# Optimization experiments

Measured on AMD Instinct MI355X. Metric: run time of the kernel, lower is better.

The kernel has to match this reference:

```python
import jax, jax.numpy as jnp
import numpy as np

B, N, F, W, D, LAT = 512, 200, 16, 256, 5, 128
ALPHA = 0.2  # tf.nn.leaky_relu default alpha


def _he_uniform(key, shape):
    fan_in = shape[-2]
    lim = np.sqrt(6.0 / fan_in)
    return jax.random.uniform(key, shape, jnp.float32, -lim, lim)


def setup_inputs() -> dict:
    key = jax.random.key(0)
    ks = jax.random.split(key, 16)
    x = jax.random.normal(ks[0], (B, N, F), jnp.float32)
    lengths = jax.random.randint(ks[1], (B,), 1, N + 1)
    valid = (jnp.arange(N)[None, :] < lengths[:, None])[..., None]  # [B,N,1]
    x = x * valid  # zero-pad tail -> Keras Masking marks it masked
    return {
        "x": x,
        "Gamma0": _he_uniform(ks[2], (F, W)),
        "Lambda0": _he_uniform(ks[3], (F, W)),
        "Gmid": _he_uniform(ks[4], (D - 2, W, W)),
        "Lmid": _he_uniform(ks[5], (D - 2, W, W)),
        "GammaL": _he_uniform(ks[6], (W, LAT)),
        "LambdaL": _he_uniform(ks[7], (W, LAT)),
        "F0_W": _he_uniform(ks[8], (LAT, W)),
        "F0_b": jnp.zeros((W,), jnp.float32),
        "Fmid_W": _he_uniform(ks[9], (D - 1, W, W)),
        "Fmid_b": jnp.zeros((D - 1, W), jnp.float32),
        "Flast_W": _he_uniform(ks[10], (W, 2)),
        "Flast_b": jnp.zeros((2,), jnp.float32),
    }


def _lrelu(h):
    return jnp.where(h >= 0, h, ALPHA * h)


def reference(x, Gamma0, Lambda0, Gmid, Lmid, GammaL, LambdaL,
              F0_W, F0_b, Fmid_W, Fmid_b, Flast_W, Flast_b):
    # Keras Masking(mask_value=0): position is valid if any feature != 0
    maskf = jnp.any(x != 0, axis=-1, keepdims=True).astype(x.dtype)  # [B,N,1]
    denom = jnp.sum(maskf, axis=1, keepdims=True)                    # [B,1,1]

    def ds_layer(h, G, L):
        # equivariant layer: per-element projection minus broadcast masked-mean projection
        mean = jnp.sum(h * maskf, axis=1, keepdims=True) / denom     # [B,1,in]
        return h @ G - mean @ L                                      # [B,N,out]

    h = _lrelu(ds_layer(x, Gamma0, Lambda0))
    for i in range(Gmid.shape[0]):
        h = _lrelu(ds_layer(h, Gmid[i], Lmid[i]))
    h = _lrelu(ds_layer(h, GammaL, LambdaL))

    # adder (sum over valid positions)
    pooled = jnp.sum(h * maskf, axis=1)                              # [B,LAT]

    y = _lrelu(pooled @ F0_W + F0_b)
    for i in range(Fmid_W.shape[0]):
        y = _lrelu(y @ Fmid_W[i] + Fmid_b[i])
    return jax.nn.softmax(y @ Flast_W + Flast_b, axis=-1)            # [B,2]
```

## Files before the change

### kernel.cpp

```cpp
#include <hip/hip_runtime.h>
#include <hip/hip_fp16.h>
#include <stdint.h>

#define BB 512
#define NN 200
#define FF 16
#define WW 256
#define DD 5
#define LATD 128
#define ALPHA 0.2f

#define WS_NV   0
#define WS_PERM 2048
#define WS_WSF  4096

typedef _Float16 f16x8 __attribute__((ext_vector_type(8)));
typedef float f32x4 __attribute__((ext_vector_type(4)));

__device__ __forceinline__ float lrelu(float v) { return v >= 0.f ? v : ALPHA * v; }
__device__ __forceinline__ unsigned pk2(float a, float b) {
    __half2 h = __floats2half2_rn(a, b);
    return *reinterpret_cast<unsigned*>(&h);
}
__device__ __forceinline__ unsigned swz(int rl, int cb) {
    return (unsigned)(rl * 512 + cb) ^ (unsigned)((rl & 7) << 4);
}

__global__ __launch_bounds__(256) void k1_kernel(const float* __restrict__ x,
                                                 const float* __restrict__ Gmid,
                                                 const float* __restrict__ GammaL,
                                                 _Float16* __restrict__ wsf,
                                                 int* __restrict__ nv) {
    const int tid = threadIdx.x;
    if (blockIdx.x < BB) {
        __shared__ int wavecnt[4];
        const int lane = tid & 63, w = tid >> 6;
        const float* xb = x + (size_t)blockIdx.x * NN * FF;
        bool flag = false;
        if (tid < NN) {
            const float4* xr = (const float4*)(xb + tid * FF);
            float4 v0 = xr[0], v1 = xr[1], v2 = xr[2], v3 = xr[3];
            flag = (v0.x != 0.f) | (v0.y != 0.f) | (v0.z != 0.f) | (v0.w != 0.f) |
                   (v1.x != 0.f) | (v1.y != 0.f) | (v1.z != 0.f) | (v1.w != 0.f) |
                   (v2.x != 0.f) | (v2.y != 0.f) | (v2.z != 0.f) | (v2.w != 0.f) |
                   (v3.x != 0.f) | (v3.y != 0.f) | (v3.z != 0.f) | (v3.w != 0.f);
        }
        unsigned long long bal = __ballot(flag);
        if (lane == 0) wavecnt[w] = __popcll(bal);
        __syncthreads();
        if (tid == 0) nv[blockIdx.x] = wavecnt[0] + wavecnt[1] + wavecnt[2] + wavecnt[3];
        return;
    }
    int t = (int)(blockIdx.x - BB) * 256 + tid;
    if (t < 24576) {
        int layer = t / 8192, r = t % 8192;
        int a = r / 256, n = r % 256;
        const float* G = Gmid + (size_t)layer * 65536;
        f16x8 v;
#pragma unroll
        for (int j = 0; j < 8; ++j) v[j] = (_Float16)G[(8 * a + j) * 256 + n];
        int chunk = a >> 2, g = a & 3, cf = n >> 4, ln = (n & 15) + 16 * g;
        *(f16x8*)(wsf + (size_t)layer * 65536 + ((size_t)(chunk * 16 + cf) * 64 + ln) * 8) = v;
    } else if (t < 28672) {
        int r = t - 24576;
        int a = r / 128, n = r % 128;
        f16x8 v;
#pragma unroll
        for (int j = 0; j < 8; ++j) v[j] = (_Float16)GammaL[(8 * a + j) * 128 + n];
        int chunk = a >> 2, g = a & 3, cf = n >> 4, ln = (n & 15) + 16 * g;
        *(f16x8*)(wsf + 196608 + ((size_t)(chunk * 8 + cf) * 64 + ln) * 8) = v;
    }
}

__global__ __launch_bounds__(512) void rank_kernel(const int* __restrict__ nv,
                                                   int* __restrict__ perm) {
    __shared__ int nvs[512];
    const int t = threadIdx.x;
    int my = nv[t];
    nvs[t] = my;
    __syncthreads();
    int rank = 0;
    for (int b2 = 0; b2 < 512; ++b2) {
        int o = nvs[b2];
        rank += (o > my) || (o == my && b2 < t);
    }
    perm[rank] = t;
}

struct __align__(16) FusedLds {
    unsigned short tile[NN * 256];
    float xl[NN * FF];
    float g0[FF * WW];
    float mred[512];
    float csred[8][256];
    float csl[256];
    float mpj_s[256];
    float ybuf[2][256];
    float xmean[FF];
    int wavecnt[8];
};

template <int NC>
__device__ __forceinline__ void colsum_finish(FusedLds& S, const float* fs,
                                              int tid, int lane, int w) {
    constexpr int CPW = NC / 64;
    const int cg = w & 3, cl = lane & 15;
#pragma unroll
    for (int u = 0; u < CPW; ++u) {
        float s = fs[u];
        s += __shfl_xor(s, 16);
        s += __shfl_xor(s, 32);
        if (lane < 16) S.csred[w][(cg * CPW + u) * 16 + cl] = s;
    }
    __syncthreads();
    if (tid < NC) {
        const int cgb = tid / (16 * CPW);
        S.csl[tid] = S.csred[cgb][tid] + S.csred[4 + cgb][tid];
    }
    __syncthreads();
}

template <int NC>
__device__ __forceinline__ void tile_layer(FusedLds& S, const _Float16* __restrict__ wf,
                                           int Nv, int tid, int lane, int w) {
    constexpr int CPW = NC / 64;
    const int rg = w >> 2, cg = w & 3, cl = lane & 15, g = lane >> 4;
    const int RFL = (Nv + 15) >> 4;
    float fs[CPW];
#pragma unroll
    for (int u = 0; u < CPW; ++u) fs[u] = 0.f;
    for (int p0 = 0; p0 < RFL; p0 += 8) {
        f32x4 acc[4][CPW];
#pragma unroll
        for (int i = 0; i < 4; ++i)
#pragma unroll
            for (int u = 0; u < CPW; ++u)
#pragma unroll
                for (int j = 0; j < 4; ++j) acc[i][u][j] = 0.f;
        bool act[4];
        int rll[4];
#pragma unroll
        for (int i = 0; i < 4; ++i) {
            const int rf = p0 + rg + 2 * i;
            act[i] = rf < RFL;
            int rl = rf * 16 + cl;
            rll[i] = rl < Nv ? rl : Nv - 1;
        }
#pragma unroll
        for (int c = 0; c < 8; ++c) {
            f16x8 bfr[CPW];
#pragma unroll
            for (int u = 0; u < CPW; ++u)
                bfr[u] = *(const f16x8*)(wf + ((size_t)(c * (NC / 16) + cg * CPW + u) * 64 + lane) * 8);
#pragma unroll
            for (int i = 0; i < 4; ++i) {
                if (act[i]) {
                    f16x8 af = *(const f16x8*)((const char*)S.tile + swz(rll[i], c * 64 + (g << 4)));
#pragma unroll
                    for (int u = 0; u < CPW; ++u)
                        acc[i][u] = __builtin_amdgcn_mfma_f32_16x16x32_f16(af, bfr[u], acc[i][u], 0, 0, 0);
                }
            }
        }
        __syncthreads();
#pragma unroll
        for (int i = 0; i < 4; ++i) {
            if (act[i]) {
                const int rlb = (p0 + rg + 2 * i) * 16 + 4 * g;
#pragma unroll
                for (int j = 0; j < 4; ++j) {
                    const int rl = rlb + j;
                    if (rl < Nv) {
#pragma unroll
                        for (int u = 0; u < CPW; ++u) {
                            const int col = (cg * CPW + u) * 16 + cl;
                            float o = lrelu(acc[i][u][j] - S.mpj_s[col]);
                            *(_Float16*)((char*)S.tile + swz(rl, col * 2)) = (_Float16)o;
                            fs[u] += o;
                        }
                    }
                }
            }
        }
        __syncthreads();
    }
    colsum_finish<NC>(S, fs, tid, lane, w);
}

__device__ __forceinline__ void mproj_mid(FusedLds& S, const float* __restrict__ Lmid,
                                          int l, float invNv, int tid) {
    const float* L = Lmid + (size_t)l * 65536;
    const int c = tid & 255, seg = tid >> 8;
    float a = 0.f;
    const float* Lp = L + (size_t)seg * 128 * 256 + c;
    const float* mh = S.csl + seg * 128;
#pragma unroll 8
    for (int k = 0; k < 128; ++k) a = fmaf(mh[k], Lp[(size_t)k * 256], a);
    S.mred[seg * 256 + c] = a;
    __syncthreads();
    if (tid < 256) S.mpj_s[tid] = (S.mred[tid] + S.mred[256 + tid]) * invNv;
    __syncthreads();
}

__device__ __forceinline__ void mproj_last(FusedLds& S, const float* __restrict__ LambdaL,
                                           float invNv, int tid) {
    const int c = tid & 127, seg = tid >> 7;
    float a = 0.f;
    const float* Lp = LambdaL + (size_t)seg * 64 * 128 + c;
    const float* mh = S.csl + seg * 64;
#pragma unroll 8
    for (int k = 0; k < 64; ++k) a = fmaf(mh[k], Lp[(size_t)k * 128], a);
    S.mred[seg * 128 + c] = a;
    __syncthreads();
    if (tid < 128)
        S.mpj_s[tid] = (S.mred[tid] + S.mred[128 + tid] + S.mred[256 + tid] + S.mred[384 + tid]) * invNv;
    __syncthreads();
}

__global__ __launch_bounds__(512, 2) void fused_kernel(
    const float* __restrict__ x,
    const float* __restrict__ Gamma0, const float* __restrict__ Lambda0,
    const float* __restrict__ Lmid, const float* __restrict__ LambdaL,
    const float* __restrict__ F0W, const float* __restrict__ F0b,
    const float* __restrict__ FmidW, const float* __restrict__ Fmidb,
    const float* __restrict__ FlastW, const float* __restrict__ Flastb,
    const int* __restrict__ perm, const _Float16* __restrict__ wsf,
    float* __restrict__ out) {
    __shared__ FusedLds S;
    const int tid = threadIdx.x, lane = tid & 63, w = tid >> 6;
    const int b = perm[blockIdx.x];
    const float* xb = x + (size_t)b * NN * FF;

    ((float4*)S.g0)[tid] = ((const float4*)Gamma0)[tid];
    ((float4*)S.g0)[tid + 512] = ((const float4*)Gamma0)[tid + 512];
    float4 v0, v1, v2, v3;
    bool flag = false;
    if (tid < NN) {
        const float4* xr = (const float4*)(xb + tid * FF);
        v0 = xr[0]; v1 = xr[1]; v2 = xr[2]; v3 = xr[3];
        flag = (v0.x != 0.f) | (v0.y != 0.f) | (v0.z != 0.f) | (v0.w != 0.f) |
               (v1.x != 0.f) | (v1.y != 0.f) | (v1.z != 0.f) | (v1.w != 0.f) |
               (v2.x != 0.f) | (v2.y != 0.f) | (v2.z != 0.f) | (v2.w != 0.f) |
               (v3.x != 0.f) | (v3.y != 0.f) | (v3.z != 0.f) | (v3.w != 0.f);
    }
    unsigned long long bal = __ballot(flag);
    if (lane == 0) S.wavecnt[w] = __popcll(bal);
    {
        int n0 = tid >> 4, f = tid & 15;
        float a = 0.f;
        for (int n = n0; n < NN; n += 32) a += xb[n * FF + f];
        S.mred[n0 * 16 + f] = a;
    }
    __syncthreads();
    int basec = 0, tot = 0;
#pragma unroll
    for (int w2 = 0; w2 < 8; ++w2) {
        int c = S.wavecnt[w2];
        if (w2 < w) basec += c;
        tot += c;
    }
    const int Nv = tot;
    const float invNv = 1.0f / (float)Nv;
    if (flag) {
        int pos = basec + __popcll(bal & ((1ull << lane) - 1ull));
        float4* dst = (float4*)&S.xl[pos * FF];
        dst[0] = v0; dst[1] = v1; dst[2] = v2; dst[3] = v3;
    }
    if (tid < FF) {
        float s = 0.f;
#pragma unroll
        for (int g2 = 0; g2 < 32; ++g2) s += S.mred[g2 * 16 + tid];
        S.xmean[tid] = s * invNv;
    }
    __syncthreads();
    if (tid < WW) {
        float a = 0.f;
#pragma unroll
        for (int f = 0; f < FF; ++f) a = fmaf(S.xmean[f], Lambda0[f * WW + tid], a);
        S.mpj_s[tid] = a;
    }
    __syncthreads();

    {
        const float4 mp = *(const float4*)&S.mpj_s[4 * lane];
        float p[4] = {0.f, 0.f, 0.f, 0.f};
        for (int r = w; r < Nv; r += 8) {
            float acc[4] = {0.f, 0.f, 0.f, 0.f};
#pragma unroll
            for (int f = 0; f < FF; ++f) {
                float xv = S.xl[r * FF + f];
                float4 gv = *(const float4*)&S.g0[f * WW + 4 * lane];
                acc[0] = fmaf(xv, gv.x, acc[0]);
                acc[1] = fmaf(xv, gv.y, acc[1]);
                acc[2] = fmaf(xv, gv.z, acc[2]);
                acc[3] = fmaf(xv, gv.w, acc[3]);
            }
            float o0 = lrelu(acc[0] - mp.x), o1 = lrelu(acc[1] - mp.y);
            float o2 = lrelu(acc[2] - mp.z), o3 = lrelu(acc[3] - mp.w);
            uint2 ov;
            ov.x = pk2(o0, o1);
            ov.y = pk2(o2, o3);
            *(uint2*)((char*)S.tile + swz(r, 8 * lane)) = ov;
            p[0] += o0; p[1] += o1; p[2] += o2; p[3] += o3;
        }
        __syncthreads();
#pragma unroll
        for (int c4 = 0; c4 < 4; ++c4) S.csred[w][4 * lane + c4] = p[c4];
        __syncthreads();
        if (tid < 256) {
            float s = 0.f;
#pragma unroll
            for (int w2 = 0; w2 < 8; ++w2) s += S.csred[w2][tid];
            S.csl[tid] = s;
        }
        __syncthreads();
    }

    for (int l = 0; l < DD - 2; ++l) {
        mproj_mid(S, Lmid, l, invNv, tid);
        tile_layer<256>(S, wsf + (size_t)l * 65536, Nv, tid, lane, w);
    }
    mproj_last(S, LambdaL, invNv, tid);
    tile_layer<128>(S, wsf + 196608, Nv, tid, lane, w);

    {
        const int c = tid & 255, seg = tid >> 8;
        float a = 0.f;
        const float* Wp = F0W + (size_t)seg * 64 * WW + c;
        const float* ip = S.csl + seg * 64;
#pragma unroll
        for (int k = 0; k < 64; ++k) a = fmaf(ip[k], Wp[(size_t)k * WW], a);
        S.mred[seg * WW + c] = a;
        __syncthreads();
        if (tid < WW) S.ybuf[0][tid] = lrelu(S.mred[tid] + S.mred[WW + tid] + F0b[tid]);
        __syncthreads();
    }
    int cur = 0;
    for (int i = 0; i < DD - 1; ++i) {
        const int c = tid & 255, seg = tid >> 8;
        const float* Wp = FmidW + (size_t)i * WW * WW + (size_t)seg * 128 * WW + c;
        const float* ip = S.ybuf[cur] + seg * 128;
        float a = 0.f;
#pragma unroll
        for (int k = 0; k < 128; ++k) a = fmaf(ip[k], Wp[(size_t)k * WW], a);
        S.mred[seg * WW + c] = a;
        __syncthreads();
        if (tid < WW)
            S.ybuf[1 - cur][tid] = lrelu(S.mred[tid] + S.mred[WW + tid] + Fmidb[i * WW + tid]);
        __syncthreads();
        cur = 1 - cur;
    }
    if (w == 0) {
        float s0 = 0.f, s1 = 0.f;
        for (int k = lane; k < WW; k += 64) {
            float yv = S.ybuf[cur][k];
            s0 = fmaf(yv, FlastW[2 * k], s0);
            s1 = fmaf(yv, FlastW[2 * k + 1], s1);
        }
#pragma unroll
        for (int off = 32; off > 0; off >>= 1) {
            s0 += __shfl_down(s0, off);
            s1 += __shfl_down(s1, off);
        }
        if (lane == 0) {
            s0 += Flastb[0];
            s1 += Flastb[1];
            float m = fmaxf(s0, s1);
            float e0 = expf(s0 - m), e1 = expf(s1 - m);
            float inv = 1.0f / (e0 + e1);
            out[2 * b] = e0 * inv;
            out[2 * b + 1] = e1 * inv;
        }
    }
}

extern "C" void kernel_launch(void* const* d_in, const int* in_sizes, int n_in,
                              void* d_out, int out_size, void* d_ws, size_t ws_size,
                              hipStream_t stream) {
    const float* x = (const float*)d_in[0];
    const float* Gamma0 = (const float*)d_in[1];
    const float* Lambda0 = (const float*)d_in[2];
    const float* Gmid = (const float*)d_in[3];
    const float* Lmid = (const float*)d_in[4];
    const float* GammaL = (const float*)d_in[5];
    const float* LambdaL = (const float*)d_in[6];
    const float* F0W = (const float*)d_in[7];
    const float* F0b = (const float*)d_in[8];
    const float* FmidW = (const float*)d_in[9];
    const float* Fmidb = (const float*)d_in[10];
    const float* FlastW = (const float*)d_in[11];
    const float* Flastb = (const float*)d_in[12];
    float* out = (float*)d_out;

    int* nvb = (int*)((char*)d_ws + WS_NV);
    int* perm = (int*)((char*)d_ws + WS_PERM);
    _Float16* wsf = (_Float16*)((char*)d_ws + WS_WSF);

    k1_kernel<<<BB + 112, 256, 0, stream>>>(x, Gmid, GammaL, wsf, nvb);
    rank_kernel<<<1, 512, 0, stream>>>(nvb, perm);
    fused_kernel<<<BB, 512, 0, stream>>>(x, Gamma0, Lambda0, Lmid, LambdaL,
                                         F0W, F0b, FmidW, Fmidb, FlastW, Flastb,
                                         perm, wsf, out);
}
```

Measured before the change: 147.8 us.

## Double fused block to 1024 threads and cover all rows in one MFMA pass

```diff
diff --git a/kernel.cpp b/kernel.cpp
--- a/kernel.cpp
+++ b/kernel.cpp
@@ -9,6 +9,7 @@
 #define DD 5
 #define LATD 128
 #define ALPHA 0.2f
+#define NT 1024
 
 #define WS_NV   0
 #define WS_PERM 2048
@@ -89,15 +90,16 @@
 
 struct __align__(16) FusedLds {
     unsigned short tile[NN * 256];
-    float xl[NN * FF];
-    float g0[FF * WW];
-    float mred[512];
-    float csred[8][256];
+    union U {
+        struct { float xl[NN * FF]; float g0[FF * WW]; } p;
+        float csred[16][256];
+    } u;
+    float mred[1024];
     float csl[256];
     float mpj_s[256];
     float ybuf[2][256];
     float xmean[FF];
-    int wavecnt[8];
+    int wavecnt[16];
 };
 
 template <int NC>
@@ -110,12 +112,13 @@
         float s = fs[u];
         s += __shfl_xor(s, 16);
         s += __shfl_xor(s, 32);
-        if (lane < 16) S.csred[w][(cg * CPW + u) * 16 + cl] = s;
+        if (lane < 16) S.u.csred[w][(cg * CPW + u) * 16 + cl] = s;
     }
     __syncthreads();
     if (tid < NC) {
         const int cgb = tid / (16 * CPW);
-        S.csl[tid] = S.csred[cgb][tid] + S.csred[4 + cgb][tid];
+        S.csl[tid] = S.u.csred[cgb][tid] + S.u.csred[4 + cgb][tid] +
+                     S.u.csred[8 + cgb][tid] + S.u.csred[12 + cgb][tid];
     }
     __syncthreads();
 }
@@ -129,60 +132,57 @@
     float fs[CPW];
 #pragma unroll
     for (int u = 0; u < CPW; ++u) fs[u] = 0.f;
-    for (int p0 = 0; p0 < RFL; p0 += 8) {
-        f32x4 acc[4][CPW];
-#pragma unroll
-        for (int i = 0; i < 4; ++i)
-#pragma unroll
-            for (int u = 0; u < CPW; ++u)
-#pragma unroll
-                for (int j = 0; j < 4; ++j) acc[i][u][j] = 0.f;
-        bool act[4];
-        int rll[4];
-#pragma unroll
-        for (int i = 0; i < 4; ++i) {
-            const int rf = p0 + rg + 2 * i;
-            act[i] = rf < RFL;
-            int rl = rf * 16 + cl;
-            rll[i] = rl < Nv ? rl : Nv - 1;
-        }
-#pragma unroll
-        for (int c = 0; c < 8; ++c) {
-            f16x8 bfr[CPW];
-#pragma unroll
-            for (int u = 0; u < CPW; ++u)
-                bfr[u] = *(const f16x8*)(wf + ((size_t)(c * (NC / 16) + cg * CPW + u) * 64 + lane) * 8);
-#pragma unroll
-            for (int i = 0; i < 4; ++i) {
-                if (act[i]) {
-                    f16x8 af = *(const f16x8*)((const char*)S.tile + swz(rll[i], c * 64 + (g << 4)));
-#pragma unroll
-                    for (int u = 0; u < CPW; ++u)
-                        acc[i][u] = __builtin_amdgcn_mfma_f32_16x16x32_f16(af, bfr[u], acc[i][u], 0, 0, 0);
-                }
-            }
-        }
-        __syncthreads();
+    f32x4 acc[4][CPW];
+#pragma unroll
+    for (int i = 0; i < 4; ++i)
+#pragma unroll
+        for (int u = 0; u < CPW; ++u)
+#pragma unroll
+            for (int j = 0; j < 4; ++j) acc[i][u][j] = 0.f;
+    bool act[4];
+    int rll[4];
+#pragma unroll
+    for (int i = 0; i < 4; ++i) {
+        const int rf = rg + 4 * i;
+        act[i] = rf < RFL;
+        int rl = rf * 16 + cl;
+        rll[i] = rl < Nv ? rl : Nv - 1;
+    }
+#pragma unroll
+    for (int c = 0; c < 8; ++c) {
+        f16x8 bfr[CPW];
+#pragma unroll
+        for (int u = 0; u < CPW; ++u)
+            bfr[u] = *(const f16x8*)(wf + ((size_t)(c * (NC / 16) + cg * CPW + u) * 64 + lane) * 8);
 #pragma unroll
         for (int i = 0; i < 4; ++i) {
             if (act[i]) {
-                const int rlb = (p0 + rg + 2 * i) * 16 + 4 * g;
-#pragma unroll
-                for (int j = 0; j < 4; ++j) {
-                    const int rl = rlb + j;
-                    if (rl < Nv) {
-#pragma unroll
-                        for (int u = 0; u < CPW; ++u) {
-                            const int col = (cg * CPW + u) * 16 + cl;
-                            float o = lrelu(acc[i][u][j] - S.mpj_s[col]);
-                            *(_Float16*)((char*)S.tile + swz(rl, col * 2)) = (_Float16)o;
-                            fs[u] += o;
-                        }
+                f16x8 af = *(const f16x8*)((const char*)S.tile + swz(rll[i], c * 64 + (g << 4)));
+#pragma unroll
+                for (int u = 0; u < CPW; ++u)
+                    acc[i][u] = __builtin_amdgcn_mfma_f32_16x16x32_f16(af, bfr[u], acc[i][u], 0, 0, 0);
+            }
+        }
+    }
+    __syncthreads();
+#pragma unroll
+    for (int i = 0; i < 4; ++i) {
+        if (act[i]) {
+            const int rlb = (rg + 4 * i) * 16 + 4 * g;
+#pragma unroll
+            for (int j = 0; j < 4; ++j) {
+                const int rl = rlb + j;
+                if (rl < Nv) {
+#pragma unroll
+                    for (int u = 0; u < CPW; ++u) {
+                        const int col = (cg * CPW + u) * 16 + cl;
+                        float o = lrelu(acc[i][u][j] - S.mpj_s[col]);
+                        *(_Float16*)((char*)S.tile + swz(rl, col * 2)) = (_Float16)o;
+                        fs[u] += o;
                     }
                 }
             }
         }
-        __syncthreads();
     }
     colsum_finish<NC>(S, fs, tid, lane, w);
 }
@@ -192,13 +192,14 @@
     const float* L = Lmid + (size_t)l * 65536;
     const int c = tid & 255, seg = tid >> 8;
     float a = 0.f;
-    const float* Lp = L + (size_t)seg * 128 * 256 + c;
-    const float* mh = S.csl + seg * 128;
+    const float* Lp = L + (size_t)seg * 64 * 256 + c;
+    const float* mh = S.csl + seg * 64;
 #pragma unroll 8
-    for (int k = 0; k < 128; ++k) a = fmaf(mh[k], Lp[(size_t)k * 256], a);
+    for (int k = 0; k < 64; ++k) a = fmaf(mh[k], Lp[(size_t)k * 256], a);
     S.mred[seg * 256 + c] = a;
     __syncthreads();
-    if (tid < 256) S.mpj_s[tid] = (S.mred[tid] + S.mred[256 + tid]) * invNv;
+    if (tid < 256)
+        S.mpj_s[tid] = (S.mred[tid] + S.mred[256 + tid] + S.mred[512 + tid] + S.mred[768 + tid]) * invNv;
     __syncthreads();
 }
 
@@ -206,18 +207,22 @@
                                            float invNv, int tid) {
     const int c = tid & 127, seg = tid >> 7;
     float a = 0.f;
-    const float* Lp = LambdaL + (size_t)seg * 64 * 128 + c;
-    const float* mh = S.csl + seg * 64;
+    const float* Lp = LambdaL + (size_t)seg * 32 * 128 + c;
+    const float* mh = S.csl + seg * 32;
 #pragma unroll 8
-    for (int k = 0; k < 64; ++k) a = fmaf(mh[k], Lp[(size_t)k * 128], a);
+    for (int k = 0; k < 32; ++k) a = fmaf(mh[k], Lp[(size_t)k * 128], a);
     S.mred[seg * 128 + c] = a;
     __syncthreads();
-    if (tid < 128)
-        S.mpj_s[tid] = (S.mred[tid] + S.mred[128 + tid] + S.mred[256 + tid] + S.mred[384 + tid]) * invNv;
-    __syncthreads();
-}
-
-__global__ __launch_bounds__(512, 2) void fused_kernel(
+    if (tid < 128) {
+        float s = 0.f;
+#pragma unroll
+        for (int q = 0; q < 8; ++q) s += S.mred[q * 128 + tid];
+        S.mpj_s[tid] = s * invNv;
+    }
+    __syncthreads();
+}
+
+__global__ __launch_bounds__(NT, 2) void fused_kernel(
     const float* __restrict__ x,
     const float* __restrict__ Gamma0, const float* __restrict__ Lambda0,
     const float* __restrict__ Lmid, const float* __restrict__ LambdaL,
@@ -231,8 +236,7 @@
     const int b = perm[blockIdx.x];
     const float* xb = x + (size_t)b * NN * FF;
 
-    ((float4*)S.g0)[tid] = ((const float4*)Gamma0)[tid];
-    ((float4*)S.g0)[tid + 512] = ((const float4*)Gamma0)[tid + 512];
+    ((float4*)S.u.p.g0)[tid] = ((const float4*)Gamma0)[tid];
     float4 v0, v1, v2, v3;
     bool flag = false;
     if (tid < NN) {
@@ -248,13 +252,13 @@
     {
         int n0 = tid >> 4, f = tid & 15;
         float a = 0.f;
-        for (int n = n0; n < NN; n += 32) a += xb[n * FF + f];
+        for (int n = n0; n < NN; n += 64) a += xb[n * FF + f];
         S.mred[n0 * 16 + f] = a;
     }
     __syncthreads();
     int basec = 0, tot = 0;
 #pragma unroll
-    for (int w2 = 0; w2 < 8; ++w2) {
+    for (int w2 = 0; w2 < 16; ++w2) {
         int c = S.wavecnt[w2];
         if (w2 < w) basec += c;
         tot += c;
@@ -263,13 +267,13 @@
     const float invNv = 1.0f / (float)Nv;
     if (flag) {
         int pos = basec + __popcll(bal & ((1ull << lane) - 1ull));
-        float4* dst = (float4*)&S.xl[pos * FF];
+        float4* dst = (float4*)&S.u.p.xl[pos * FF];
         dst[0] = v0; dst[1] = v1; dst[2] = v2; dst[3] = v3;
     }
     if (tid < FF) {
         float s = 0.f;
 #pragma unroll
-        for (int g2 = 0; g2 < 32; ++g2) s += S.mred[g2 * 16 + tid];
+        for (int g2 = 0; g2 < 64; ++g2) s += S.mred[g2 * 16 + tid];
         S.xmean[tid] = s * invNv;
     }
     __syncthreads();
@@ -284,12 +288,12 @@
     {
         const float4 mp = *(const float4*)&S.mpj_s[4 * lane];
         float p[4] = {0.f, 0.f, 0.f, 0.f};
-        for (int r = w; r < Nv; r += 8) {
+        for (int r = w; r < Nv; r += 16) {
             float acc[4] = {0.f, 0.f, 0.f, 0.f};
 #pragma unroll
             for (int f = 0; f < FF; ++f) {
-                float xv = S.xl[r * FF + f];
-                float4 gv = *(const float4*)&S.g0[f * WW + 4 * lane];
+                float xv = S.u.p.xl[r * FF + f];
+                float4 gv = *(const float4*)&S.u.p.g0[f * WW + 4 * lane];
                 acc[0] = fmaf(xv, gv.x, acc[0]);
                 acc[1] = fmaf(xv, gv.y, acc[1]);
                 acc[2] = fmaf(xv, gv.z, acc[2]);
@@ -305,12 +309,12 @@
         }
         __syncthreads();
 #pragma unroll
-        for (int c4 = 0; c4 < 4; ++c4) S.csred[w][4 * lane + c4] = p[c4];
+        for (int c4 = 0; c4 < 4; ++c4) S.u.csred[w][4 * lane + c4] = p[c4];
         __syncthreads();
         if (tid < 256) {
             float s = 0.f;
 #pragma unroll
-            for (int w2 = 0; w2 < 8; ++w2) s += S.csred[w2][tid];
+            for (int w2 = 0; w2 < 16; ++w2) s += S.u.csred[w2][tid];
             S.csl[tid] = s;
         }
         __syncthreads();
@@ -326,27 +330,30 @@
     {
         const int c = tid & 255, seg = tid >> 8;
         float a = 0.f;
-        const float* Wp = F0W + (size_t)seg * 64 * WW + c;
-        const float* ip = S.csl + seg * 64;
-#pragma unroll
-        for (int k = 0; k < 64; ++k) a = fmaf(ip[k], Wp[(size_t)k * WW], a);
+        const float* Wp = F0W + (size_t)seg * 32 * WW + c;
+        const float* ip = S.csl + seg * 32;
+#pragma unroll
+        for (int k = 0; k < 32; ++k) a = fmaf(ip[k], Wp[(size_t)k * WW], a);
         S.mred[seg * WW + c] = a;
         __syncthreads();
-        if (tid < WW) S.ybuf[0][tid] = lrelu(S.mred[tid] + S.mred[WW + tid] + F0b[tid]);
+        if (tid < WW)
+            S.ybuf[0][tid] = lrelu(S.mred[tid] + S.mred[WW + tid] + S.mred[2 * WW + tid] +
+                                   S.mred[3 * WW + tid] + F0b[tid]);
         __syncthreads();
     }
     int cur = 0;
     for (int i = 0; i < DD - 1; ++i) {
         const int c = tid & 255, seg = tid >> 8;
-        const float* Wp = FmidW + (size_t)i * WW * WW + (size_t)seg * 128 * WW + c;
-        const float* ip = S.ybuf[cur] + seg * 128;
+        const float* Wp = FmidW + (size_t)i * WW * WW + (size_t)seg * 64 * WW + c;
+        const float* ip = S.ybuf[cur] + seg * 64;
         float a = 0.f;
 #pragma unroll
-        for (int k = 0; k < 128; ++k) a = fmaf(ip[k], Wp[(size_t)k * WW], a);
+        for (int k = 0; k < 64; ++k) a = fmaf(ip[k], Wp[(size_t)k * WW], a);
         S.mred[seg * WW + c] = a;
         __syncthreads();
         if (tid < WW)
-            S.ybuf[1 - cur][tid] = lrelu(S.mred[tid] + S.mred[WW + tid] + Fmidb[i * WW + tid]);
+            S.ybuf[1 - cur][tid] = lrelu(S.mred[tid] + S.mred[WW + tid] + S.mred[2 * WW + tid] +
+                                         S.mred[3 * WW + tid] + Fmidb[i * WW + tid]);
         __syncthreads();
         cur = 1 - cur;
     }
@@ -398,7 +405,7 @@
 
     k1_kernel<<<BB + 112, 256, 0, stream>>>(x, Gmid, GammaL, wsf, nvb);
     rank_kernel<<<1, 512, 0, stream>>>(nvb, perm);
-    fused_kernel<<<BB, 512, 0, stream>>>(x, Gamma0, Lambda0, Lmid, LambdaL,
-                                         F0W, F0b, FmidW, Fmidb, FlastW, Flastb,
-                                         perm, wsf, out);
-}
+    fused_kernel<<<BB, NT, 0, stream>>>(x, Gamma0, Lambda0, Lmid, LambdaL,
+                                        F0W, F0b, FmidW, Fmidb, FlastW, Flastb,
+                                        perm, wsf, out);
+}
```

Result: slower. 258.9 us (+75.2%).
